# Kernel optimization log

Measured on AMD Instinct MI355X. Metric: run time of the kernel, lower is better.

Reference implementation:

```python
import jax, jax.numpy as jnp
import numpy as np

N_HEAD = 4


def setup_inputs() -> dict:
    key = jax.random.key(0)
    ks = jax.random.split(key, 6)
    c = 256
    std = 1.0 / np.sqrt(c).astype(np.float32)
    x = jax.random.normal(ks[0], (2, c, 16, 64, 64), jnp.float32)
    Wq = jax.random.normal(ks[1], (3, c, c), jnp.float32) * std
    Wk = jax.random.normal(ks[2], (3, c, c), jnp.float32) * std
    Wv = jax.random.normal(ks[3], (3, c, c), jnp.float32) * std
    Wo = jax.random.normal(ks[4], (3, c, c), jnp.float32) * std  # n_layer=1 -> std 1/sqrt(c)
    bo = jax.random.uniform(ks[5], (3, c), jnp.float32, minval=-std, maxval=std)
    return {"x": x, "Wq": Wq, "Wk": Wk, "Wv": Wv, "Wo": Wo, "bo": bo}


def _axial_mha(h, Wq, Wk, Wv, Wo, bo, axis, n_head):
    # h: [b, d1, ..., dn, c]; attention along spatial dim `axis` (0-indexed)
    lead = h.shape[:-1]
    c = h.shape[-1]
    dk = c // n_head

    def proj_split(t, W):
        y = jnp.einsum('...c,oc->...o', t, W)          # torch Linear: x @ W^T
        y = y.reshape(t.shape[:-1] + (n_head, dk))
        return jnp.moveaxis(y, -2, 1)                  # [b, nh, d1..dn, dk]

    q = proj_split(h, Wq)
    k = proj_split(h, Wk)
    v = proj_split(h, Wv)

    ax = axis + 2  # account for batch + head dims
    q = jnp.moveaxis(q, ax, -2)
    k = jnp.moveaxis(k, ax, -2)
    v = jnp.moveaxis(v, ax, -2)

    scale = 1.0 / jnp.sqrt(jnp.asarray(dk, q.dtype))
    attn = jnp.einsum('...ld,...md->...lm', q, k) * scale
    attn = jax.nn.softmax(attn, axis=-1)
    o = jnp.einsum('...lm,...md->...ld', attn, v)

    o = jnp.moveaxis(o, -2, ax)                        # restore axis position
    o = jnp.moveaxis(o, 1, -2).reshape(lead + (c,))    # combine heads
    return jnp.einsum('...c,oc->...o', o, Wo) + bo


def reference(x, Wq, Wk, Wv, Wo, bo):
    # x: [b, c, d1, d2, d3]
    n_dims = x.ndim - 2
    h = jnp.moveaxis(x, 1, -1)  # [b, d1, d2, d3, c]
    out = jnp.zeros_like(h)
    for d in range(n_dims):
        out = out + _axial_mha(h, Wq[d], Wk[d], Wv[d], Wo[d], bo[d], d, N_HEAD)
    return jnp.moveaxis(out, -1, 1)
```

## Files before the change

kernel.cpp:

```cpp
#include <hip/hip_runtime.h>
#include <stdint.h>

typedef __attribute__((ext_vector_type(8))) short bf16x8;
typedef __attribute__((ext_vector_type(4))) short short4v;
typedef __attribute__((ext_vector_type(4))) float f32x4;

#define CCH  256
#define PSP  65536
#define NTOK 131072

static __device__ __forceinline__ short f2bf(float f) {
  union { float f; uint32_t u; } v; v.f = f;
  uint32_t r = (v.u + 0x7FFFu + ((v.u >> 16) & 1u)) >> 16;
  return (short)(uint16_t)r;
}
static __device__ __forceinline__ float bf2f(short s) {
  union { uint32_t u; float f; } v; v.u = ((uint32_t)(uint16_t)s) << 16;
  return v.f;
}

__device__ __forceinline__ void gload16(const void* g, void* l) {
  __builtin_amdgcn_global_load_lds((const __attribute__((address_space(1))) void*)g,
                                   (__attribute__((address_space(3))) void*)l,
                                   16, 0, 0);
}

__global__ __launch_bounds__(256) void k_cvt_w(const float* __restrict__ src,
                                               short* __restrict__ dst, int n) {
  int i = (blockIdx.x * 256 + threadIdx.x) * 4;
  if (i + 3 < n) {
    f32x4 v = *(const f32x4*)(src + i);
    short4v o;
    o[0] = f2bf(v[0]); o[1] = f2bf(v[1]); o[2] = f2bf(v[2]); o[3] = f2bf(v[3]);
    *(short4v*)(dst + i) = o;
  }
}

__global__ __launch_bounds__(256) void k_cvt_stackw(const float* __restrict__ src,
                                                    short* __restrict__ dst, int matoff) {
  int i = (blockIdx.x * 256 + threadIdx.x) * 4;
  if (i < 196608) {
    int ax = i >> 16;
    int rem = i & 65535;
    f32x4 v = *(const f32x4*)(src + i);
    short4v o;
    o[0] = f2bf(v[0]); o[1] = f2bf(v[1]); o[2] = f2bf(v[2]); o[3] = f2bf(v[3]);
    *(short4v*)(dst + ax * 196608 + matoff + rem) = o;
  }
}

__global__ __launch_bounds__(256) void k_tin(const float* __restrict__ x,
                                             short* __restrict__ hb) {
  __shared__ float tile[64][65];
  int p0 = blockIdx.x * 64, c0 = blockIdx.y * 64, b = blockIdx.z;
  int tid = threadIdx.x;
  int tx = tid & 63, tr = tid >> 6;
  const float* xp = x + ((size_t)b * CCH + c0) * PSP + p0;
  #pragma unroll
  for (int it = 0; it < 16; ++it) {
    int c = it * 4 + tr;
    tile[c][tx] = xp[(size_t)c * PSP + tx];
  }
  __syncthreads();
  short* hp = hb + ((size_t)b * PSP + p0) * CCH + c0;
  #pragma unroll
  for (int it = 0; it < 4; ++it) {
    int slot = it * 256 + tid;
    int p = slot >> 4, c4 = (slot & 15) * 4;
    short4v o;
    #pragma unroll
    for (int k = 0; k < 4; ++k) o[k] = f2bf(tile[c4 + k][p]);
    *(short4v*)(hp + (size_t)p * CCH + c4) = o;
  }
}

__global__ __launch_bounds__(256) void k_gemm(const short* __restrict__ hb,
    const short* __restrict__ wqkv,
    short* __restrict__ qb, short* __restrict__ kb, short* __restrict__ vb)
{
  __shared__ short sm[2][8192];
  int tid = threadIdx.x, lane = tid & 63, w = tid >> 6, g = lane >> 4, lm = lane & 15;
  int bm = blockIdx.x, bn = blockIdx.y;
  size_t m0 = (size_t)bm * 128;
  int n0 = bn * 128;
  int wtok = (w >> 1) * 64, wco = (w & 1) * 64;

  f32x4 acc[4][4];
  #pragma unroll
  for (int i = 0; i < 4; ++i)
    #pragma unroll
    for (int j = 0; j < 4; ++j) { acc[i][j][0]=0.f; acc[i][j][1]=0.f; acc[i][j][2]=0.f; acc[i][j][3]=0.f; }

  const short* Ag = hb + m0 * 256;
  const short* Bg = wqkv + (size_t)n0 * 256;

  #pragma unroll
  for (int kt = 0; kt < 4; ++kt) {
    int k0 = kt * 64;
    #pragma unroll
    for (int q = 0; q < 4; ++q) {
      int s = (w * 4 + q) * 64 + lane;
      int row = s >> 3, ch = s & 7;
      int sc = ch ^ (row & 7);
      gload16(Ag + (size_t)row * 256 + k0 + sc * 8, &sm[0][(w * 4 + q) * 512]);
    }
    #pragma unroll
    for (int q = 0; q < 4; ++q) {
      int s = (w * 4 + q) * 64 + lane;
      int row = s >> 3, ch = s & 7;
      int sc = ch ^ (row & 7);
      gload16(Bg + (size_t)row * 256 + k0 + sc * 8, &sm[1][(w * 4 + q) * 512]);
    }
    __syncthreads();
    #pragma unroll
    for (int ks = 0; ks < 2; ++ks) {
      bf16x8 af[4], bfr[4];
      #pragma unroll
      for (int i = 0; i < 4; ++i) {
        int r = wco + i * 16 + lm;
        af[i] = *(const bf16x8*)(&sm[1][r * 64 + (((ks * 4 + g) ^ (r & 7)) * 8)]);
      }
      #pragma unroll
      for (int j = 0; j < 4; ++j) {
        int r = wtok + j * 16 + lm;
        bfr[j] = *(const bf16x8*)(&sm[0][r * 64 + (((ks * 4 + g) ^ (r & 7)) * 8)]);
      }
      #pragma unroll
      for (int i = 0; i < 4; ++i)
        #pragma unroll
        for (int j = 0; j < 4; ++j)
          acc[i][j] = __builtin_amdgcn_mfma_f32_16x16x32_bf16(af[i], bfr[j], acc[i][j], 0, 0, 0);
    }
    __syncthreads();
  }

  short* ct = &sm[0][0];
  #pragma unroll
  for (int i = 0; i < 4; ++i) {
    int co = wco + i * 16 + g * 4;
    int chunk = co >> 3, off = co & 7;
    #pragma unroll
    for (int j = 0; j < 4; ++j) {
      int row = wtok + j * 16 + lm;
      short4v o;
      o[0] = f2bf(acc[i][j][0]); o[1] = f2bf(acc[i][j][1]);
      o[2] = f2bf(acc[i][j][2]); o[3] = f2bf(acc[i][j][3]);
      *(short4v*)(ct + row * 128 + ((chunk ^ (row & 7)) * 8) + off) = o;
    }
  }
  __syncthreads();

  int mat = bn >> 1;
  short* dmat = (mat == 0) ? qb : (mat == 1) ? kb : vb;
  int cbase = (bn & 1) * 128;
  #pragma unroll
  for (int it = 0; it < 8; ++it) {
    int idx = it * 256 + tid;
    int row = idx >> 4, ch = idx & 15;
    bf16x8 v = *(const bf16x8*)(ct + row * 128 + (((ch & 8) | ((ch & 7) ^ (row & 7))) * 8));
    *(bf16x8*)(dmat + (m0 + row) * 256 + cbase + ch * 8) = v;
  }
}

template<int L>
__global__ __launch_bounds__(256) void k_att(const short* __restrict__ qb,
    const short* __restrict__ kb, const short* __restrict__ vb,
    const short* __restrict__ wo, short* __restrict__ ob,
    int mulA, int mulB, int stride, int rmw)
{
  constexpr int NI = L / 16;
  constexpr int KS = (L == 64) ? 2 : 1;
  constexpr int VBYTES = 4 * L * 72 * 2;
  constexpr int OBYTES = L * 264 * 2;
  __shared__ char lds[(VBYTES > OBYTES) ? VBYTES : OBYTES];

  int tid = threadIdx.x, lane = tid & 63, w = tid >> 6, g = lane >> 4, lm = lane & 15;
  int s = blockIdx.x, b = blockIdx.y;
  size_t base = (size_t)b * PSP + (size_t)(s >> 6) * mulA + (size_t)(s & 63) * mulB;

  short* vw = (short*)lds + w * L * 72;
  if (L == 64) {
    const short* vrow = vb + (base + (size_t)lane * stride) * 256 + w * 64;
    #pragma unroll
    for (int j = 0; j < 8; ++j)
      *(bf16x8*)&vw[lane * 72 + j * 8] = *(const bf16x8*)(vrow + j * 8);
  } else {
    const short* vrow = vb + (base + (size_t)lm * stride) * 256 + w * 64 + g * 16;
    #pragma unroll
    for (int j = 0; j < 2; ++j)
      *(bf16x8*)&vw[lm * 72 + g * 16 + j * 8] = *(const bf16x8*)(vrow + j * 8);
  }
  __syncthreads();

  const short* qh = qb + base * 256 + w * 64;
  const short* kh = kb + base * 256 + w * 64;
  f32x4 t[NI][NI];
  #pragma unroll
  for (int i = 0; i < NI; ++i)
    #pragma unroll
    for (int j = 0; j < NI; ++j) { t[i][j][0]=0.f; t[i][j][1]=0.f; t[i][j][2]=0.f; t[i][j][3]=0.f; }
  #pragma unroll
  for (int ks = 0; ks < 2; ++ks) {
    bf16x8 af[NI], bq[NI];
    #pragma unroll
    for (int i = 0; i < NI; ++i)
      af[i] = *(const bf16x8*)(kh + (size_t)(i * 16 + lm) * stride * 256 + ks * 32 + g * 8);
    #pragma unroll
    for (int i = 0; i < NI; ++i)
      bq[i] = *(const bf16x8*)(qh + (size_t)(i * 16 + lm) * stride * 256 + ks * 32 + g * 8);
    #pragma unroll
    for (int mi = 0; mi < NI; ++mi)
      #pragma unroll
      for (int lj = 0; lj < NI; ++lj)
        t[mi][lj] = __builtin_amdgcn_mfma_f32_16x16x32_bf16(af[mi], bq[lj], t[mi][lj], 0, 0, 0);
  }

  const float fac = 0.18033688011112042f;
  float inv[NI];
  #pragma unroll
  for (int lj = 0; lj < NI; ++lj) {
    float mx = -3.0e38f;
    #pragma unroll
    for (int mi = 0; mi < NI; ++mi)
      #pragma unroll
      for (int r = 0; r < 4; ++r) mx = fmaxf(mx, t[mi][lj][r]);
    mx = fmaxf(mx, __shfl_xor(mx, 16));
    mx = fmaxf(mx, __shfl_xor(mx, 32));
    float sm = 0.f;
    #pragma unroll
    for (int mi = 0; mi < NI; ++mi)
      #pragma unroll
      for (int r = 0; r < 4; ++r) {
        float e = exp2f((t[mi][lj][r] - mx) * fac);
        t[mi][lj][r] = e; sm += e;
      }
    sm += __shfl_xor(sm, 16);
    sm += __shfl_xor(sm, 32);
    inv[lj] = 1.0f / sm;
  }

  bf16x8 pa[NI][KS];
  #pragma unroll
  for (int lj = 0; lj < NI; ++lj)
    #pragma unroll
    for (int ks = 0; ks < KS; ++ks) {
      bf16x8 a;
      #pragma unroll
      for (int j = 0; j < 8; ++j) {
        int mi = ks * 2 + (j >> 2);
        float v = (mi < NI) ? t[mi][lj][j & 3] * inv[lj] : 0.f;
        a[j] = f2bf(v);
      }
      pa[lj][ks] = a;
    }

  f32x4 oa[NI][4];
  #pragma unroll
  for (int i = 0; i < NI; ++i)
    #pragma unroll
    for (int j = 0; j < 4; ++j) { oa[i][j][0]=0.f; oa[i][j][1]=0.f; oa[i][j][2]=0.f; oa[i][j][3]=0.f; }
  #pragma unroll
  for (int ks = 0; ks < KS; ++ks)
    #pragma unroll
    for (int ej = 0; ej < 4; ++ej) {
      bf16x8 bv;
      int e = ej * 16 + lm;
      int rb = ks * 32 + g * 4;
      #pragma unroll
      for (int j = 0; j < 4; ++j) bv[j] = vw[(rb + j) * 72 + e];
      if (L == 64) {
        #pragma unroll
        for (int j = 0; j < 4; ++j) bv[4 + j] = vw[(rb + 16 + j) * 72 + e];
      } else {
        #pragma unroll
        for (int j = 0; j < 4; ++j) bv[4 + j] = 0;
      }
      #pragma unroll
      for (int lj = 0; lj < NI; ++lj)
        oa[lj][ej] = __builtin_amdgcn_mfma_f32_16x16x32_bf16(pa[lj][ks], bv, oa[lj][ej], 0, 0, 0);
    }

  __syncthreads();
  short* ot = (short*)lds;
  #pragma unroll
  for (int lj = 0; lj < NI; ++lj)
    #pragma unroll
    for (int ej = 0; ej < 4; ++ej)
      #pragma unroll
      for (int r = 0; r < 4; ++r)
        ot[(lj * 16 + g * 4 + r) * 264 + w * 64 + ej * 16 + lm] = f2bf(oa[lj][ej][r]);
  __syncthreads();

  constexpr int NIF = (L == 64) ? 16 : 4;
  int if0 = (L == 64) ? 0 : (w * 4);
  int tw  = (L == 64) ? (w * 16) : 0;
  f32x4 pacc[NIF];
  #pragma unroll
  for (int i = 0; i < NIF; ++i) { pacc[i][0]=0.f; pacc[i][1]=0.f; pacc[i][2]=0.f; pacc[i][3]=0.f; }
  #pragma unroll
  for (int ks = 0; ks < 8; ++ks) {
    bf16x8 bo_ = *(const bf16x8*)&ot[(tw + lm) * 264 + ks * 32 + g * 8];
    #pragma unroll
    for (int i = 0; i < NIF; ++i) {
      bf16x8 af = *(const bf16x8*)(wo + (size_t)((if0 + i) * 16 + lm) * 256 + ks * 32 + g * 8);
      pacc[i] = __builtin_amdgcn_mfma_f32_16x16x32_bf16(af, bo_, pacc[i], 0, 0, 0);
    }
  }
  size_t tokr = base + (size_t)(tw + lm) * stride;
  short* dst0 = ob + tokr * 256;
  #pragma unroll
  for (int i = 0; i < NIF; ++i) {
    int co = (if0 + i) * 16 + g * 4;
    float v0 = pacc[i][0], v1 = pacc[i][1], v2 = pacc[i][2], v3 = pacc[i][3];
    if (rmw) {
      short4v old = *(short4v*)(dst0 + co);
      v0 += bf2f(old[0]); v1 += bf2f(old[1]); v2 += bf2f(old[2]); v3 += bf2f(old[3]);
    }
    short4v o;
    o[0] = f2bf(v0); o[1] = f2bf(v1); o[2] = f2bf(v2); o[3] = f2bf(v3);
    *(short4v*)(dst0 + co) = o;
  }
}

__global__ __launch_bounds__(256) void k_final(const short* __restrict__ o0,
                                               const short* __restrict__ o1,
                                               const float* __restrict__ bo,
                                               float* __restrict__ out) {
  __shared__ float tile[64][65];
  __shared__ float bias[64];
  int p0 = blockIdx.x * 64, c0 = blockIdx.y * 64, b = blockIdx.z;
  int tid = threadIdx.x;
  if (tid < 64)
    bias[tid] = bo[c0 + tid] + bo[256 + c0 + tid] + bo[512 + c0 + tid];
  const short* a0 = o0 + ((size_t)b * PSP + p0) * CCH + c0;
  const short* a1 = o1 + ((size_t)b * PSP + p0) * CCH + c0;
  #pragma unroll
  for (int it = 0; it < 4; ++it) {
    int slot = it * 256 + tid;
    int p = slot >> 4, c4 = (slot & 15) * 4;
    short4v v0 = *(const short4v*)(a0 + (size_t)p * CCH + c4);
    short4v v1 = *(const short4v*)(a1 + (size_t)p * CCH + c4);
    #pragma unroll
    for (int j = 0; j < 4; ++j)
      tile[c4 + j][p] = bf2f(v0[j]) + bf2f(v1[j]);
  }
  __syncthreads();
  float* op = out + ((size_t)b * CCH + c0) * PSP + p0;
  int tx = tid & 63, tr = tid >> 6;
  #pragma unroll
  for (int it = 0; it < 16; ++it) {
    int c = it * 4 + tr;
    op[(size_t)c * PSP + tx] = tile[c][tx] + bias[c];
  }
}

extern "C" void kernel_launch(void* const* d_in, const int* in_sizes, int n_in,
                              void* d_out, int out_size, void* d_ws, size_t ws_size,
                              hipStream_t stream) {
  const float* x  = (const float*)d_in[0];
  const float* Wq = (const float*)d_in[1];
  const float* Wk = (const float*)d_in[2];
  const float* Wv = (const float*)d_in[3];
  const float* Wo = (const float*)d_in[4];
  const float* bo = (const float*)d_in[5];
  float* out = (float*)d_out;

  char* ws = (char*)d_ws;
  size_t off = 0;
  auto alloc = [&](size_t bytes) -> char* {
    char* p = ws + off;
    off += (bytes + 255) & ~(size_t)255;
    return p;
  };
  short* wqkv = (short*)alloc((size_t)3 * 196608 * 2);
  short* wob  = (short*)alloc((size_t)3 * 65536 * 2);
  short* hb   = (short*)alloc((size_t)NTOK * 256 * 2);
  short* qbuf = (short*)alloc((size_t)NTOK * 256 * 2);
  short* kbuf = (short*)alloc((size_t)NTOK * 256 * 2);
  short* vbuf = (short*)alloc((size_t)NTOK * 256 * 2);
  short* o0   = (short*)alloc((size_t)NTOK * 256 * 2);
  short* o1   = (short*)alloc((size_t)NTOK * 256 * 2);
  if (off > ws_size) return;

  k_cvt_stackw<<<192, 256, 0, stream>>>(Wq, wqkv, 0);
  k_cvt_stackw<<<192, 256, 0, stream>>>(Wk, wqkv, 65536);
  k_cvt_stackw<<<192, 256, 0, stream>>>(Wv, wqkv, 131072);
  k_cvt_w<<<192, 256, 0, stream>>>(Wo, wob, 196608);
  k_tin<<<dim3(1024, 4, 2), 256, 0, stream>>>(x, hb);

  for (int ax = 0; ax < 3; ++ax) {
    k_gemm<<<dim3(1024, 6), 256, 0, stream>>>(hb, wqkv + (size_t)ax * 196608,
                                              qbuf, kbuf, vbuf);
    if (ax == 0)
      k_att<16><<<dim3(4096, 2), 256, 0, stream>>>(qbuf, kbuf, vbuf, wob, o0,
                                                   64, 1, 4096, 0);
    else if (ax == 1)
      k_att<64><<<dim3(1024, 2), 256, 0, stream>>>(qbuf, kbuf, vbuf, wob + 65536, o1,
                                                   4096, 1, 64, 0);
    else
      k_att<64><<<dim3(1024, 2), 256, 0, stream>>>(qbuf, kbuf, vbuf, wob + 131072, o1,
                                                   4096, 64, 1, 1);
  }
  k_final<<<dim3(1024, 4, 2), 256, 0, stream>>>(o0, o1, bo, out);
}
```

Measured before the change: 1.107 ms.

## Restructure axial attention kernel: prefetch Q/K with V, transpose PV, split Wo by output channel

The V tile, the first Q/K slice and the LDS store of V are now issued before any MFMA, and the barrier after the V staging is removed, so global load latency overlaps. The PV product is computed transposed (V fragment as the A operand), which allows 4-element vector stores of the O tile to LDS. The output projection now gives each wave a 64-channel slice of Wo across all tokens instead of all channels for a token slice, so Wo global reads are spread across waves. The trade-off is higher register pressure from the prefetched fragments and the larger accumulator array.

```diff
diff --git a/kernel.cpp b/kernel.cpp
--- a/kernel.cpp
+++ b/kernel.cpp
@@ -170,6 +170,7 @@
 {
   constexpr int NI = L / 16;
   constexpr int KS = (L == 64) ? 2 : 1;
+  constexpr int NV = (L == 64) ? 8 : 2;
   constexpr int VBYTES = 4 * L * 72 * 2;
   constexpr int OBYTES = L * 264 * 2;
   __shared__ char lds[(VBYTES > OBYTES) ? VBYTES : OBYTES];
@@ -179,40 +180,58 @@
   size_t base = (size_t)b * PSP + (size_t)(s >> 6) * mulA + (size_t)(s & 63) * mulB;
 
   short* vw = (short*)lds + w * L * 72;
+
+  bf16x8 vr[NV];
   if (L == 64) {
     const short* vrow = vb + (base + (size_t)lane * stride) * 256 + w * 64;
     #pragma unroll
-    for (int j = 0; j < 8; ++j)
-      *(bf16x8*)&vw[lane * 72 + j * 8] = *(const bf16x8*)(vrow + j * 8);
+    for (int j = 0; j < NV; ++j) vr[j] = *(const bf16x8*)(vrow + j * 8);
   } else {
     const short* vrow = vb + (base + (size_t)lm * stride) * 256 + w * 64 + g * 16;
     #pragma unroll
-    for (int j = 0; j < 2; ++j)
-      *(bf16x8*)&vw[lm * 72 + g * 16 + j * 8] = *(const bf16x8*)(vrow + j * 8);
-  }
-  __syncthreads();
-
+    for (int j = 0; j < NV; ++j) vr[j] = *(const bf16x8*)(vrow + j * 8);
+  }
   const short* qh = qb + base * 256 + w * 64;
   const short* kh = kb + base * 256 + w * 64;
+  bf16x8 af0[NI], bq0[NI];
+  #pragma unroll
+  for (int i = 0; i < NI; ++i)
+    af0[i] = *(const bf16x8*)(kh + (size_t)(i * 16 + lm) * stride * 256 + g * 8);
+  #pragma unroll
+  for (int i = 0; i < NI; ++i)
+    bq0[i] = *(const bf16x8*)(qh + (size_t)(i * 16 + lm) * stride * 256 + g * 8);
+
+  if (L == 64) {
+    #pragma unroll
+    for (int j = 0; j < NV; ++j) *(bf16x8*)&vw[lane * 72 + j * 8] = vr[j];
+  } else {
+    #pragma unroll
+    for (int j = 0; j < NV; ++j) *(bf16x8*)&vw[lm * 72 + g * 16 + j * 8] = vr[j];
+  }
+
   f32x4 t[NI][NI];
   #pragma unroll
   for (int i = 0; i < NI; ++i)
     #pragma unroll
     for (int j = 0; j < NI; ++j) { t[i][j][0]=0.f; t[i][j][1]=0.f; t[i][j][2]=0.f; t[i][j][3]=0.f; }
   #pragma unroll
-  for (int ks = 0; ks < 2; ++ks) {
-    bf16x8 af[NI], bq[NI];
+  for (int mi = 0; mi < NI; ++mi)
+    #pragma unroll
+    for (int lj = 0; lj < NI; ++lj)
+      t[mi][lj] = __builtin_amdgcn_mfma_f32_16x16x32_bf16(af0[mi], bq0[lj], t[mi][lj], 0, 0, 0);
+  {
+    bf16x8 af1[NI], bq1[NI];
     #pragma unroll
     for (int i = 0; i < NI; ++i)
-      af[i] = *(const bf16x8*)(kh + (size_t)(i * 16 + lm) * stride * 256 + ks * 32 + g * 8);
+      af1[i] = *(const bf16x8*)(kh + (size_t)(i * 16 + lm) * stride * 256 + 32 + g * 8);
     #pragma unroll
     for (int i = 0; i < NI; ++i)
-      bq[i] = *(const bf16x8*)(qh + (size_t)(i * 16 + lm) * stride * 256 + ks * 32 + g * 8);
+      bq1[i] = *(const bf16x8*)(qh + (size_t)(i * 16 + lm) * stride * 256 + 32 + g * 8);
     #pragma unroll
     for (int mi = 0; mi < NI; ++mi)
       #pragma unroll
       for (int lj = 0; lj < NI; ++lj)
-        t[mi][lj] = __builtin_amdgcn_mfma_f32_16x16x32_bf16(af[mi], bq[lj], t[mi][lj], 0, 0, 0);
+        t[mi][lj] = __builtin_amdgcn_mfma_f32_16x16x32_bf16(af1[mi], bq1[lj], t[mi][lj], 0, 0, 0);
   }
 
   const float fac = 0.18033688011112042f;
@@ -239,7 +258,7 @@
     inv[lj] = 1.0f / sm;
   }
 
-  bf16x8 pa[NI][KS];
+  bf16x8 pb[NI][KS];
   #pragma unroll
   for (int lj = 0; lj < NI; ++lj)
     #pragma unroll
@@ -251,74 +270,80 @@
         float v = (mi < NI) ? t[mi][lj][j & 3] * inv[lj] : 0.f;
         a[j] = f2bf(v);
       }
-      pa[lj][ks] = a;
-    }
-
-  f32x4 oa[NI][4];
-  #pragma unroll
-  for (int i = 0; i < NI; ++i)
-    #pragma unroll
-    for (int j = 0; j < 4; ++j) { oa[i][j][0]=0.f; oa[i][j][1]=0.f; oa[i][j][2]=0.f; oa[i][j][3]=0.f; }
+      pb[lj][ks] = a;
+    }
+
+  f32x4 oa[4][NI];
+  #pragma unroll
+  for (int ej = 0; ej < 4; ++ej)
+    #pragma unroll
+    for (int lj = 0; lj < NI; ++lj) { oa[ej][lj][0]=0.f; oa[ej][lj][1]=0.f; oa[ej][lj][2]=0.f; oa[ej][lj][3]=0.f; }
   #pragma unroll
   for (int ks = 0; ks < KS; ++ks)
     #pragma unroll
     for (int ej = 0; ej < 4; ++ej) {
-      bf16x8 bv;
-      int e = ej * 16 + lm;
-      int rb = ks * 32 + g * 4;
-      #pragma unroll
-      for (int j = 0; j < 4; ++j) bv[j] = vw[(rb + j) * 72 + e];
-      if (L == 64) {
-        #pragma unroll
-        for (int j = 0; j < 4; ++j) bv[4 + j] = vw[(rb + 16 + j) * 72 + e];
-      } else {
-        #pragma unroll
-        for (int j = 0; j < 4; ++j) bv[4 + j] = 0;
+      bf16x8 vf;
+      #pragma unroll
+      for (int j = 0; j < 8; ++j) {
+        if (L == 16 && j >= 4) { vf[j] = 0; }
+        else {
+          int row = ks * 32 + 16 * (j >> 2) + 4 * g + (j & 3);
+          vf[j] = vw[row * 72 + ej * 16 + lm];
+        }
       }
       #pragma unroll
       for (int lj = 0; lj < NI; ++lj)
-        oa[lj][ej] = __builtin_amdgcn_mfma_f32_16x16x32_bf16(pa[lj][ks], bv, oa[lj][ej], 0, 0, 0);
+        oa[ej][lj] = __builtin_amdgcn_mfma_f32_16x16x32_bf16(vf, pb[lj][ks], oa[ej][lj], 0, 0, 0);
     }
 
   __syncthreads();
   short* ot = (short*)lds;
   #pragma unroll
-  for (int lj = 0; lj < NI; ++lj)
-    #pragma unroll
-    for (int ej = 0; ej < 4; ++ej)
-      #pragma unroll
-      for (int r = 0; r < 4; ++r)
-        ot[(lj * 16 + g * 4 + r) * 264 + w * 64 + ej * 16 + lm] = f2bf(oa[lj][ej][r]);
+  for (int ej = 0; ej < 4; ++ej)
+    #pragma unroll
+    for (int lj = 0; lj < NI; ++lj) {
+      short4v o;
+      #pragma unroll
+      for (int r = 0; r < 4; ++r) o[r] = f2bf(oa[ej][lj][r]);
+      *(short4v*)&ot[(lj * 16 + lm) * 264 + w * 64 + ej * 16 + g * 4] = o;
+    }
   __syncthreads();
 
-  constexpr int NIF = (L == 64) ? 16 : 4;
-  int if0 = (L == 64) ? 0 : (w * 4);
-  int tw  = (L == 64) ? (w * 16) : 0;
-  f32x4 pacc[NIF];
-  #pragma unroll
-  for (int i = 0; i < NIF; ++i) { pacc[i][0]=0.f; pacc[i][1]=0.f; pacc[i][2]=0.f; pacc[i][3]=0.f; }
+  f32x4 pacc[4][NI];
+  #pragma unroll
+  for (int i = 0; i < 4; ++i)
+    #pragma unroll
+    for (int j = 0; j < NI; ++j) { pacc[i][j][0]=0.f; pacc[i][j][1]=0.f; pacc[i][j][2]=0.f; pacc[i][j][3]=0.f; }
   #pragma unroll
   for (int ks = 0; ks < 8; ++ks) {
-    bf16x8 bo_ = *(const bf16x8*)&ot[(tw + lm) * 264 + ks * 32 + g * 8];
-    #pragma unroll
-    for (int i = 0; i < NIF; ++i) {
-      bf16x8 af = *(const bf16x8*)(wo + (size_t)((if0 + i) * 16 + lm) * 256 + ks * 32 + g * 8);
-      pacc[i] = __builtin_amdgcn_mfma_f32_16x16x32_bf16(af, bo_, pacc[i], 0, 0, 0);
-    }
-  }
-  size_t tokr = base + (size_t)(tw + lm) * stride;
-  short* dst0 = ob + tokr * 256;
-  #pragma unroll
-  for (int i = 0; i < NIF; ++i) {
-    int co = (if0 + i) * 16 + g * 4;
-    float v0 = pacc[i][0], v1 = pacc[i][1], v2 = pacc[i][2], v3 = pacc[i][3];
-    if (rmw) {
-      short4v old = *(short4v*)(dst0 + co);
-      v0 += bf2f(old[0]); v1 += bf2f(old[1]); v2 += bf2f(old[2]); v3 += bf2f(old[3]);
-    }
-    short4v o;
-    o[0] = f2bf(v0); o[1] = f2bf(v1); o[2] = f2bf(v2); o[3] = f2bf(v3);
-    *(short4v*)(dst0 + co) = o;
+    bf16x8 bfr[NI];
+    #pragma unroll
+    for (int j = 0; j < NI; ++j)
+      bfr[j] = *(const bf16x8*)&ot[(j * 16 + lm) * 264 + ks * 32 + g * 8];
+    #pragma unroll
+    for (int i = 0; i < 4; ++i) {
+      bf16x8 afr = *(const bf16x8*)(wo + (size_t)(w * 64 + i * 16 + lm) * 256 + ks * 32 + g * 8);
+      #pragma unroll
+      for (int j = 0; j < NI; ++j)
+        pacc[i][j] = __builtin_amdgcn_mfma_f32_16x16x32_bf16(afr, bfr[j], pacc[i][j], 0, 0, 0);
+    }
+  }
+  #pragma unroll
+  for (int j = 0; j < NI; ++j) {
+    size_t tokr = base + (size_t)(j * 16 + lm) * stride;
+    short* dst0 = ob + tokr * 256 + w * 64;
+    #pragma unroll
+    for (int i = 0; i < 4; ++i) {
+      int co = i * 16 + g * 4;
+      float v0 = pacc[i][j][0], v1 = pacc[i][j][1], v2 = pacc[i][j][2], v3 = pacc[i][j][3];
+      if (rmw) {
+        short4v old = *(short4v*)(dst0 + co);
+        v0 += bf2f(old[0]); v1 += bf2f(old[1]); v2 += bf2f(old[2]); v3 += bf2f(old[3]);
+      }
+      short4v o;
+      o[0] = f2bf(v0); o[1] = f2bf(v1); o[2] = f2bf(v2); o[3] = f2bf(v3);
+      *(short4v*)(dst0 + co) = o;
+    }
   }
 }
 
```

After: 933.7 us. 15.7% less time.
